# Optimization experiments

Hardware: AMD Instinct MI355X
Metric: run time of the kernel (lower is better)

## Reference

```python
import jax, jax.numpy as jnp
import numpy as np

INPUT_SIZE = 1024
HIDDEN_SIZE = 1024
W_RANK = 64
U_RANK = 64
BATCH = 32768


def setup_inputs() -> dict:
    key = jax.random.key(0)
    ks = jax.random.split(key, 16)
    p = lambda k, shape: 0.1 * jax.random.normal(k, shape, dtype=jnp.float32)
    return {
        "x": jax.random.normal(ks[0], (BATCH, INPUT_SIZE), dtype=jnp.float32),
        "h": jax.random.normal(ks[1], (BATCH, HIDDEN_SIZE), dtype=jnp.float32),
        "W": p(ks[2], (INPUT_SIZE, W_RANK)),
        "W1": p(ks[3], (W_RANK, HIDDEN_SIZE)),
        "W2": p(ks[4], (W_RANK, HIDDEN_SIZE)),
        "W3": p(ks[5], (W_RANK, HIDDEN_SIZE)),
        "U": p(ks[6], (HIDDEN_SIZE, U_RANK)),
        "U1": p(ks[7], (U_RANK, HIDDEN_SIZE)),
        "U2": p(ks[8], (U_RANK, HIDDEN_SIZE)),
        "U3": p(ks[9], (U_RANK, HIDDEN_SIZE)),
        "U1_diag": p(ks[10], (HIDDEN_SIZE,)),
        "U2_diag": p(ks[11], (HIDDEN_SIZE,)),
        "U3_diag": p(ks[12], (HIDDEN_SIZE,)),
        "bias_r": jnp.ones((1, HIDDEN_SIZE), dtype=jnp.float32),
        "bias_gate": jnp.ones((1, HIDDEN_SIZE), dtype=jnp.float32),
        "bias_update": jnp.ones((1, HIDDEN_SIZE), dtype=jnp.float32),
    }


def reference(x, h, W, W1, W2, W3, U, U1, U2, U3,
              U1_diag, U2_diag, U3_diag, bias_r, bias_gate, bias_update):
    # Low-rank projections shared across gates (matches torch matmul order)
    xW = x @ W          # [B, wRank]
    hU = h @ U          # [B, uRank]
    wVal1 = xW @ W1
    wVal2 = xW @ W2
    wVal3 = xW @ W3
    uVal1 = hU @ U1
    uVal2 = hU @ U2
    r = jax.nn.sigmoid(wVal1 + uVal1 + h * U1_diag + bias_r)
    z = jax.nn.sigmoid(wVal2 + uVal2 + h * U2_diag + bias_gate)
    rh = r * h
    matVal_c = wVal3 + (rh @ U) @ U3 + rh * U3_diag
    c_tilda = jnp.tanh(matVal_c + bias_update)
    h_next = z * h + (1.0 - z) * c_tilda
    return h_next
```

## Files before the change

### kernel.cpp

```cpp
#include <hip/hip_runtime.h>
#include <hip/hip_bf16.h>


typedef __attribute__((ext_vector_type(8))) short short8;
typedef __attribute__((ext_vector_type(4))) float f32x4;
typedef __attribute__((ext_vector_type(4))) float f4;

#define WS_UT   65536
#define WS_P1T  131072
#define WS_P2T  262144
#define WS_P3T  393216
#define WS_A12  524288
#define WS_RHU  4718592

__device__ __forceinline__ short f2bf(float f) {
  unsigned u = __builtin_bit_cast(unsigned, f);
  u += 0x7FFFu + ((u >> 16) & 1u);
  return (short)(u >> 16);
}
__device__ __forceinline__ short8 cvt8(f4 a, f4 b) {
  short8 r;
#pragma unroll
  for (int j = 0; j < 4; ++j) { r[j] = f2bf(a[j]); r[4 + j] = f2bf(b[j]); }
  return r;
}
__device__ __forceinline__ f32x4 mfma16(short8 a, short8 b, f32x4 c) {
  return __builtin_amdgcn_mfma_f32_16x16x32_bf16(a, b, c, 0, 0, 0);
}
__device__ __forceinline__ short8 ldg8(const short* p) {
  return *reinterpret_cast<const short8*>(p);
}
__device__ __forceinline__ f4 ldf4(const float* p) {
  return *reinterpret_cast<const f4*>(p);
}

__device__ __forceinline__ void cp16(void* l, const void* g) {
  __builtin_amdgcn_global_load_lds(
      (const __attribute__((address_space(1))) void*)g,
      (__attribute__((address_space(3))) void*)l, 16, 0, 0);
}
#define VWAIT(N) do { asm volatile("s_waitcnt vmcnt(" #N ")" ::: "memory"); \
                      __builtin_amdgcn_sched_barrier(0); } while (0)

__device__ __forceinline__ short8 rd128s(const short* b, int row, int col) {
  return *reinterpret_cast<const short8*>(b + row * 128 + (col ^ ((row & 7) << 3)));
}
__device__ __forceinline__ void wr128s(short* b, int row, int col8, short8 v) {
  *reinterpret_cast<short8*>(b + row * 128 + (col8 ^ ((row & 7) << 3))) = v;
}
__device__ __forceinline__ void wr64(short* b, int row, int col, short v) {
  b[row * 64 + (col ^ ((row & 7) << 3))] = v;
}
__device__ __forceinline__ short8 rd64(const short* b, int row, int col) {
  return *reinterpret_cast<const short8*>(b + row * 64 + (col ^ ((row & 7) << 3)));
}

#define LOG2E 1.4426950408889634f
__device__ __forceinline__ float sigm_f(float v) {
  return __builtin_amdgcn_rcpf(1.f + __builtin_amdgcn_exp2f(-v * LOG2E));
}
__device__ __forceinline__ float tanh_f(float v) {
  float t = __builtin_amdgcn_exp2f(v * (2.f * LOG2E));
  return 1.f - 2.f * __builtin_amdgcn_rcpf(t + 1.f);
}

__global__ void prep_kernel(const float* __restrict__ W,  const float* __restrict__ W1,
                            const float* __restrict__ W2, const float* __restrict__ W3,
                            const float* __restrict__ U,  const float* __restrict__ U1,
                            const float* __restrict__ U2, const float* __restrict__ U3,
                            short* __restrict__ ws) {
  int i = blockIdx.x * blockDim.x + threadIdx.x;
  float v;
  if (i < 65536) {
    int n = i >> 10, k = i & 1023;
    v = W[k * 64 + n];
  } else if (i < 131072) {
    int j = i - 65536;
    int n = j >> 10, k = j & 1023;
    v = U[k * 64 + n];
  } else {
    int j = i - 131072;
    int sel = j >> 17;
    int jj = j & 131071;
    int n = jj >> 7, k = jj & 127;
    const float* Wk = sel == 0 ? W1 : sel == 1 ? W2 : W3;
    const float* Uk = sel == 0 ? U1 : sel == 1 ? U2 : U3;
    v = (k < 64) ? Wk[k * 1024 + n] : Uk[(k - 64) * 1024 + n];
  }
  ws[i] = f2bf(v);
}

__global__ __launch_bounds__(256, 4) void k1_a12(
    const float* __restrict__ x, const float* __restrict__ h,
    const short* __restrict__ ws, short* __restrict__ A12) {
  __shared__ __align__(16) float sS[2][4][16 * 64];

  const int tid = threadIdx.x;
  const int w = tid >> 6, l = tid & 63, l15 = l & 15, lg = l >> 4;
  const int m = w >> 1, half = w & 1;
  const int sr = blockIdx.x * 32 + half * 16;
  const float* src = m ? h : x;
  const short* Bt  = ws + m * WS_UT;

  const int srow = l >> 4;
  const int slin = (l & 15) * 16;

  auto STAGE = [&](int c, int b) {
#pragma unroll
    for (int i = 0; i < 4; ++i) {
      int r = i * 4 + srow;
      int kb = slin ^ ((r & 7) << 4);
      cp16((char*)&sS[b][w][0] + i * 1024,
           (const char*)(src + (size_t)(sr + r) * 1024 + c * 64) + kb);
    }
  };
  auto WLOAD = [&](int c, short8* bw) {
#pragma unroll
    for (int ks = 0; ks < 2; ++ks)
#pragma unroll
      for (int cf = 0; cf < 4; ++cf)
        bw[ks * 4 + cf] =
            ldg8(Bt + (size_t)(cf * 16 + l15) * 1024 + c * 64 + ks * 32 + lg * 8);
  };

  f32x4 acc[4] = {};
  short8 bwb[2][8];
  STAGE(0, 0);
  WLOAD(0, bwb[0]);
#pragma unroll
  for (int c = 0; c < 16; ++c) {
    if (c < 15) {
      WLOAD(c + 1, bwb[(c + 1) & 1]);
      STAGE(c + 1, (c + 1) & 1);
      VWAIT(12);
    } else {
      VWAIT(0);
    }
    const char* Bb = (const char*)&sS[c & 1][w][0];
    const int s = (l15 & 7) << 4;
    const short8* bw = bwb[c & 1];
#pragma unroll
    for (int ks = 0; ks < 2; ++ks) {
      const int kb0 = (ks * 32 + lg * 8) * 4;
      f4 pa = *(const f4*)(Bb + l15 * 256 + (kb0 ^ s));
      f4 pb = *(const f4*)(Bb + l15 * 256 + ((kb0 + 16) ^ s));
      short8 av = cvt8(pa, pb);
#pragma unroll
      for (int cf = 0; cf < 4; ++cf) acc[cf] = mfma16(av, bw[ks * 4 + cf], acc[cf]);
    }
  }
#pragma unroll
  for (int cf = 0; cf < 4; ++cf)
#pragma unroll
    for (int j = 0; j < 4; ++j)
      A12[(size_t)(sr + lg * 4 + j) * 128 + m * 64 + cf * 16 + l15] = f2bf(acc[cf][j]);
}

__global__ __launch_bounds__(256, 4) void k23_rhu(
    const float* __restrict__ h, const float* __restrict__ u1d,
    const float* __restrict__ biasR,
    const short* __restrict__ ws, const short* __restrict__ A12,
    short* __restrict__ rhU) {
  const short* Ut  = ws + WS_UT;
  const short* P1t = ws + WS_P1T;
  __shared__ __align__(16) short sT[4][2][16 * 64];
  __shared__ __align__(16) float sRed[2][2][16 * 64];

  const int tid = threadIdx.x;
  const int w   = tid >> 6, l = tid & 63, l15 = l & 15, lg = l >> 4;
  const int s   = w >> 1;
  const int ch  = w & 1;
  const int sr  = blockIdx.x * 32 + s * 16;

  short8 a12[4];
#pragma unroll
  for (int k0 = 0; k0 < 4; ++k0)
    a12[k0] = ldg8(A12 + (size_t)(sr + l15) * 128 + k0 * 32 + lg * 8);

  f32x4 accU[4] = {};
#pragma unroll 1
  for (int tt = 0; tt < 8; ++tt) {
    const int n0 = ch * 512 + tt * 64;

    float hv[4][4];
#pragma unroll
    for (int cf = 0; cf < 4; ++cf)
#pragma unroll
      for (int j = 0; j < 4; ++j)
        hv[cf][j] = h[(size_t)(sr + lg * 4 + j) * 1024 + n0 + cf * 16 + l15];

    f32x4 accR[4] = {};
#pragma unroll
    for (int k0 = 0; k0 < 4; ++k0)
#pragma unroll
      for (int cf = 0; cf < 4; ++cf)
        accR[cf] = mfma16(a12[k0],
            ldg8(P1t + (size_t)(n0 + cf * 16 + l15) * 128 + k0 * 32 + lg * 8),
            accR[cf]);

    short* sw = &sT[w][tt & 1][0];
#pragma unroll
    for (int cf = 0; cf < 4; ++cf) {
      const int cc = n0 + cf * 16 + l15;
      const float d1 = u1d[cc], b_r = biasR[cc];
#pragma unroll
      for (int j = 0; j < 4; ++j) {
        float rv = sigm_f(accR[cf][j] + hv[cf][j] * d1 + b_r);
        wr64(sw, lg * 4 + j, cf * 16 + l15, f2bf(rv * hv[cf][j]));
      }
    }
    short8 arh0 = rd64(sw, l15, lg * 8);
    short8 arh1 = rd64(sw, l15, 32 + lg * 8);
#pragma unroll
    for (int cf = 0; cf < 4; ++cf)
      accU[cf] = mfma16(arh0,
          ldg8(Ut + (size_t)(cf * 16 + l15) * 1024 + n0 + lg * 8), accU[cf]);
#pragma unroll
    for (int cf = 0; cf < 4; ++cf)
      accU[cf] = mfma16(arh1,
          ldg8(Ut + (size_t)(cf * 16 + l15) * 1024 + n0 + 32 + lg * 8), accU[cf]);
  }

  {
    float* fT = &sRed[s][ch][0];
#pragma unroll
    for (int cf = 0; cf < 4; ++cf)
#pragma unroll
      for (int j = 0; j < 4; ++j) {
        int row = lg * 4 + j, col = cf * 16 + l15;
        fT[row * 64 + (col ^ ((row & 7) << 2))] = accU[cf][j];
      }
  }
  __syncthreads();
  if (ch == 0) {
    const float* f0 = &sRed[s][0][0];
    const float* f1 = &sRed[s][1][0];
#pragma unroll
    for (int cf = 0; cf < 4; ++cf)
#pragma unroll
      for (int j = 0; j < 4; ++j) {
        int row = lg * 4 + j, col = cf * 16 + l15;
        int idx = row * 64 + (col ^ ((row & 7) << 2));
        rhU[(size_t)(sr + row) * 64 + col] = f2bf(f0[idx] + f1[idx]);
      }
  }
}

__global__ __launch_bounds__(256, 2) void k4_out(
    const float* __restrict__ h,
    const float* __restrict__ u1d, const float* __restrict__ u2d,
    const float* __restrict__ u3d,
    const float* __restrict__ biasR, const float* __restrict__ biasZ,
    const float* __restrict__ biasU,
    const short* __restrict__ ws, const short* __restrict__ A12,
    const short* __restrict__ rhU, float* __restrict__ out) {
  __shared__ __align__(16) short sB1[64 * 128], sB2[64 * 128], sB3[64 * 128];
  __shared__ __align__(16) float hS[2][4][16 * 64];

  const int tid = threadIdx.x;
  const int w = tid >> 6, l = tid & 63, l15 = l & 15, lg = l >> 4;
  const int ct = blockIdx.x & 15, rc = blockIdx.x >> 4;
  const int n0 = ct * 64;

#pragma unroll
  for (int mat = 0; mat < 3; ++mat) {
    const short* srcw = (mat == 0) ? (ws + WS_P1T) : (mat == 1) ? (ws + WS_P2T) : (ws + WS_P3T);
    short* dst = (mat == 0) ? sB1 : (mat == 1) ? sB2 : sB3;
#pragma unroll
    for (int i = 0; i < 4; ++i) {
      int id = tid + i * 256;
      int row = id >> 4, gc = id & 15;
      wr128s(dst, row, gc * 8, ldg8(srcw + (size_t)(n0 + row) * 128 + gc * 8));
    }
  }
  float d1_[4], d2_[4], d3_[4], br_[4], bz_[4], bu_[4];
#pragma unroll
  for (int cf = 0; cf < 4; ++cf) {
    const int cc = n0 + cf * 16 + l15;
    d1_[cf] = u1d[cc]; d2_[cf] = u2d[cc]; d3_[cf] = u3d[cc];
    br_[cf] = biasR[cc]; bz_[cf] = biasZ[cc]; bu_[cf] = biasU[cc];
  }
  __syncthreads();

  const int srow = l >> 4;
  const int slin = (l & 15) * 16;
  auto STAGE = [&](int rnd, int b) {
    const int sb = rc * 512 + rnd * 64 + w * 16;
#pragma unroll
    for (int i = 0; i < 4; ++i) {
      int r = i * 4 + srow;
      int kb = slin ^ ((r & 7) << 4);
      cp16((char*)&hS[b][w][0] + i * 1024,
           (const char*)(h + (size_t)(sb + r) * 1024 + n0) + kb);
    }
  };

  STAGE(0, 0);
#pragma unroll 1
  for (int rnd = 0; rnd < 8; ++rnd) {
    const int sr = rc * 512 + rnd * 64 + w * 16;
    short8 a12[4], arhu[2];
#pragma unroll
    for (int k0 = 0; k0 < 4; ++k0)
      a12[k0] = ldg8(A12 + (size_t)(sr + l15) * 128 + k0 * 32 + lg * 8);
#pragma unroll
    for (int kk = 0; kk < 2; ++kk)
      arhu[kk] = ldg8(rhU + (size_t)(sr + l15) * 64 + kk * 32 + lg * 8);
    if (rnd < 7) { STAGE(rnd + 1, (rnd + 1) & 1); VWAIT(4); }
    else         { VWAIT(0); }
    const char* H = (const char*)&hS[rnd & 1][w][0];

    float hv[4][4];
#pragma unroll
    for (int cf = 0; cf < 4; ++cf)
#pragma unroll
      for (int j = 0; j < 4; ++j) {
        int rr = lg * 4 + j;
        hv[cf][j] = *(const float*)(H + rr * 256 + ((cf * 64 + l15 * 4) ^ ((rr & 7) << 4)));
      }

    f32x4 aR[4] = {}, aZ[4] = {}, aC[4] = {};
#pragma unroll
    for (int k0 = 0; k0 < 4; ++k0) {
      const short8 a3 = (k0 < 2) ? a12[k0] : arhu[k0 - 2];
#pragma unroll
      for (int cf = 0; cf < 4; ++cf) {
        aR[cf] = mfma16(a12[k0], rd128s(sB1, cf * 16 + l15, k0 * 32 + lg * 8), aR[cf]);
        aZ[cf] = mfma16(a12[k0], rd128s(sB2, cf * 16 + l15, k0 * 32 + lg * 8), aZ[cf]);
        aC[cf] = mfma16(a3,      rd128s(sB3, cf * 16 + l15, k0 * 32 + lg * 8), aC[cf]);
      }
    }
#pragma unroll
    for (int cf = 0; cf < 4; ++cf) {
      const int cc = n0 + cf * 16 + l15;
#pragma unroll
      for (int j = 0; j < 4; ++j) {
        const size_t gi = (size_t)(sr + lg * 4 + j) * 1024 + cc;
        const float hvj = hv[cf][j];
        float rv = sigm_f(aR[cf][j] + hvj * d1_[cf] + br_[cf]);
        float zv = sigm_f(aZ[cf][j] + hvj * d2_[cf] + bz_[cf]);
        float cv = tanh_f(aC[cf][j] + rv * hvj * d3_[cf] + bu_[cf]);
        out[gi] = zv * hvj + (1.f - zv) * cv;
      }
    }
  }
}

extern "C" void kernel_launch(void* const* d_in, const int* in_sizes, int n_in,
                              void* d_out, int out_size, void* d_ws, size_t ws_size,
                              hipStream_t stream) {
  const float* x   = (const float*)d_in[0];
  const float* h   = (const float*)d_in[1];
  const float* W   = (const float*)d_in[2];
  const float* W1  = (const float*)d_in[3];
  const float* W2  = (const float*)d_in[4];
  const float* W3  = (const float*)d_in[5];
  const float* U   = (const float*)d_in[6];
  const float* U1  = (const float*)d_in[7];
  const float* U2  = (const float*)d_in[8];
  const float* U3  = (const float*)d_in[9];
  const float* u1d = (const float*)d_in[10];
  const float* u2d = (const float*)d_in[11];
  const float* u3d = (const float*)d_in[12];
  const float* bR  = (const float*)d_in[13];
  const float* bZ  = (const float*)d_in[14];
  const float* bU  = (const float*)d_in[15];
  short* ws  = (short*)d_ws;
  short* A12 = ws + WS_A12;
  short* rhU = ws + WS_RHU;

  prep_kernel<<<2048, 256, 0, stream>>>(W, W1, W2, W3, U, U1, U2, U3, ws);
  k1_a12<<<1024, 256, 0, stream>>>(x, h, ws, A12);
  k23_rhu<<<1024, 256, 0, stream>>>(h, u1d, bR, ws, A12, rhU);
  k4_out<<<1024, 256, 0, stream>>>(h, u1d, u2d, u3d, bR, bZ, bU, ws, A12, rhU, (float*)d_out);
}
```

Baseline: 240.7 us.

## Split K across waves in k1_a12 with LDS reduction and doubled grid

The x@W / h@U projection kernel now gives each block 16 rows instead of 32. The two waves per matrix each handle half of the K dimension, and their partial sums are combined through shared memory before the bf16 store. The grid doubles to 2048 blocks, shared memory per block halves, and launch bounds now target 8 blocks per CU, all to raise occupancy and memory-level parallelism on this bandwidth-bound read of x and h. The cost is an extra LDS reduction with two barriers and fewer MFMAs per load, since the B-operand fragments are no longer reused across two row halves.

```diff
diff --git a/kernel.cpp b/kernel.cpp
--- a/kernel.cpp
+++ b/kernel.cpp
@@ -90,41 +90,39 @@
   ws[i] = f2bf(v);
 }
 
-__global__ __launch_bounds__(256, 4) void k1_a12(
+__global__ __launch_bounds__(256, 8) void k1_a12(
     const float* __restrict__ x, const float* __restrict__ h,
     const short* __restrict__ ws, short* __restrict__ A12) {
-  __shared__ __align__(16) float sS[2][4][16 * 64];
+  __shared__ __align__(16) float sS[2][4][16 * 32];
 
   const int tid = threadIdx.x;
   const int w = tid >> 6, l = tid & 63, l15 = l & 15, lg = l >> 4;
-  const int m = w >> 1, half = w & 1;
-  const int sr = blockIdx.x * 32 + half * 16;
+  const int m = w >> 1, kh = w & 1;
+  const int sr = blockIdx.x * 16;
   const float* src = m ? h : x;
   const short* Bt  = ws + m * WS_UT;
-
-  const int srow = l >> 4;
-  const int slin = (l & 15) * 16;
+  const int kb0 = kh * 512;
+
+  const int srow = l >> 3;
+  const int slin = (l & 7) * 16;
 
   auto STAGE = [&](int c, int b) {
 #pragma unroll
-    for (int i = 0; i < 4; ++i) {
-      int r = i * 4 + srow;
+    for (int i = 0; i < 2; ++i) {
+      int r = i * 8 + srow;
       int kb = slin ^ ((r & 7) << 4);
       cp16((char*)&sS[b][w][0] + i * 1024,
-           (const char*)(src + (size_t)(sr + r) * 1024 + c * 64) + kb);
+           (const char*)(src + (size_t)(sr + r) * 1024 + kb0 + c * 32) + kb);
     }
   };
   auto WLOAD = [&](int c, short8* bw) {
 #pragma unroll
-    for (int ks = 0; ks < 2; ++ks)
-#pragma unroll
-      for (int cf = 0; cf < 4; ++cf)
-        bw[ks * 4 + cf] =
-            ldg8(Bt + (size_t)(cf * 16 + l15) * 1024 + c * 64 + ks * 32 + lg * 8);
+    for (int cf = 0; cf < 4; ++cf)
+      bw[cf] = ldg8(Bt + (size_t)(cf * 16 + l15) * 1024 + kb0 + c * 32 + lg * 8);
   };
 
   f32x4 acc[4] = {};
-  short8 bwb[2][8];
+  short8 bwb[2][4];
   STAGE(0, 0);
   WLOAD(0, bwb[0]);
 #pragma unroll
@@ -132,28 +130,39 @@
     if (c < 15) {
       WLOAD(c + 1, bwb[(c + 1) & 1]);
       STAGE(c + 1, (c + 1) & 1);
-      VWAIT(12);
+      VWAIT(6);
     } else {
       VWAIT(0);
     }
     const char* Bb = (const char*)&sS[c & 1][w][0];
     const int s = (l15 & 7) << 4;
+    f4 pa = *(const f4*)(Bb + l15 * 128 + ((lg * 32) ^ s));
+    f4 pb = *(const f4*)(Bb + l15 * 128 + ((lg * 32 + 16) ^ s));
+    short8 av = cvt8(pa, pb);
     const short8* bw = bwb[c & 1];
 #pragma unroll
-    for (int ks = 0; ks < 2; ++ks) {
-      const int kb0 = (ks * 32 + lg * 8) * 4;
-      f4 pa = *(const f4*)(Bb + l15 * 256 + (kb0 ^ s));
-      f4 pb = *(const f4*)(Bb + l15 * 256 + ((kb0 + 16) ^ s));
-      short8 av = cvt8(pa, pb);
-#pragma unroll
-      for (int cf = 0; cf < 4; ++cf) acc[cf] = mfma16(av, bw[ks * 4 + cf], acc[cf]);
-    }
-  }
-#pragma unroll
-  for (int cf = 0; cf < 4; ++cf)
-#pragma unroll
-    for (int j = 0; j < 4; ++j)
-      A12[(size_t)(sr + lg * 4 + j) * 128 + m * 64 + cf * 16 + l15] = f2bf(acc[cf][j]);
+    for (int cf = 0; cf < 4; ++cf) acc[cf] = mfma16(av, bw[cf], acc[cf]);
+  }
+
+  __syncthreads();
+  float* sP = (float*)&sS[0][0][0];
+  if (kh == 1) {
+#pragma unroll
+    for (int cf = 0; cf < 4; ++cf)
+#pragma unroll
+      for (int j = 0; j < 4; ++j)
+        sP[(m * 16 + lg * 4 + j) * 66 + cf * 16 + l15] = acc[cf][j];
+  }
+  __syncthreads();
+  if (kh == 0) {
+#pragma unroll
+    for (int cf = 0; cf < 4; ++cf)
+#pragma unroll
+      for (int j = 0; j < 4; ++j) {
+        float v = acc[cf][j] + sP[(m * 16 + lg * 4 + j) * 66 + cf * 16 + l15];
+        A12[(size_t)(sr + lg * 4 + j) * 128 + m * 64 + cf * 16 + l15] = f2bf(v);
+      }
+  }
 }
 
 __global__ __launch_bounds__(256, 4) void k23_rhu(
@@ -370,7 +379,7 @@
   short* rhU = ws + WS_RHU;
 
   prep_kernel<<<2048, 256, 0, stream>>>(W, W1, W2, W3, U, U1, U2, U3, ws);
-  k1_a12<<<1024, 256, 0, stream>>>(x, h, ws, A12);
+  k1_a12<<<2048, 256, 0, stream>>>(x, h, ws, A12);
   k23_rhu<<<1024, 256, 0, stream>>>(h, u1d, bR, ws, A12, rhU);
   k4_out<<<1024, 256, 0, stream>>>(h, u1d, u2d, u3d, bR, bZ, bU, ws, A12, rhU, (float*)d_out);
 }
```

Result: slower. 319.7 us (+32.8%).
